# Performance work log

Hardware: AMD Instinct MI355X
Metric: run time of the kernel (lower is better)

The kernel has to match this reference:

```python
import jax, jax.numpy as jnp
import numpy as np

B, H = 4096, 200
NU, NV = 100000, 100000
DU, DV = 64, 64


def setup_inputs() -> dict:
    key = jax.random.key(0)
    ks = jax.random.split(key, 16)
    s = 0.05
    return {
        "nodes": jax.random.randint(ks[0], (B,), 0, NU),
        "history_uv": jax.random.randint(ks[1], (B, H), 0, NV),
        "history_r": jax.random.uniform(ks[2], (B, H), dtype=jnp.float32),
        "u2e_w": jax.random.normal(ks[3], (NU, DU), dtype=jnp.float32) * s,
        "v2e_w": jax.random.normal(ks[4], (NV, DV), dtype=jnp.float32) * s,
        "w_r1_w": jax.random.normal(ks[5], (DV, DV + 1), dtype=jnp.float32) * s,
        "w_r1_b": jax.random.normal(ks[6], (DV,), dtype=jnp.float32) * s,
        "w_r2_w": jax.random.normal(ks[7], (DV, DV), dtype=jnp.float32) * s,
        "w_r2_b": jax.random.normal(ks[8], (DV,), dtype=jnp.float32) * s,
        "att1_w": jax.random.normal(ks[9], (DV, DV + DU), dtype=jnp.float32) * s,
        "att1_b": jax.random.normal(ks[10], (DV,), dtype=jnp.float32) * s,
        "att2_w": jax.random.normal(ks[11], (DV, DV), dtype=jnp.float32) * s,
        "att2_b": jax.random.normal(ks[12], (DV,), dtype=jnp.float32) * s,
        "att3_w": jax.random.normal(ks[13], (1, DV), dtype=jnp.float32) * s,
        "att3_b": jax.random.normal(ks[14], (1,), dtype=jnp.float32) * s,
    }


def reference(nodes, history_uv, history_r, u2e_w, v2e_w,
              w_r1_w, w_r1_b, w_r2_w, w_r2_b,
              att1_w, att1_b, att2_w, att2_b, att3_w, att3_b):
    # Gather: e_uv [B,H,DV], uv_rep [B,DU]
    e_uv = v2e_w[history_uv]
    uv_rep = u2e_w[nodes]
    # x = cat(e_uv, e_r) -> two Linear+ReLU (dropout is identity in eval)
    x = jnp.concatenate([e_uv, history_r[..., None]], axis=-1)  # [B,H,DV+1]
    x = jax.nn.relu(jnp.einsum('bhi,oi->bho', x, w_r1_w) + w_r1_b)
    o_history = jax.nn.relu(jnp.einsum('bhi,oi->bho', x, w_r2_w) + w_r2_b)  # [B,H,DV]
    # Attention MLP over cat(o_history, u_rep broadcast to neighbors)
    u_rep_b = jnp.broadcast_to(uv_rep[:, None, :], (o_history.shape[0], o_history.shape[1], uv_rep.shape[-1]))
    a = jnp.concatenate([o_history, u_rep_b], axis=-1)  # [B,H,DV+DU]
    a = jax.nn.relu(jnp.einsum('bhi,oi->bho', a, att1_w) + att1_b)
    a = jax.nn.relu(jnp.einsum('bhi,oi->bho', a, att2_w) + att2_b)
    logits = jnp.einsum('bhi,oi->bho', a, att3_w) + att3_b  # [B,H,1]
    att = jax.nn.softmax(logits, axis=1)  # softmax over neighbor axis
    # Attention-weighted neighbor sum: [B,DV]
    to_feats = jnp.sum(o_history * att, axis=1)
    return to_feats
```

## Files before the change

kernel.cpp:

```cpp
#include <hip/hip_runtime.h>
#include <hip/hip_bf16.h>
#include <math.h>

#define Bn 4096
#define Hn 200

typedef float f32x16 __attribute__((ext_vector_type(16)));
typedef short short8 __attribute__((ext_vector_type(8)));
typedef __bf16 bh8 __attribute__((ext_vector_type(8)));
typedef unsigned int u32;

#define TABW     3200000
#define BIAS_OFF 10240
#define WR_OFF   10496
#define AT3_OFF  10560
#define WTOT     10624

__device__ __forceinline__ u32 pk2(float a, float b){
    union { __hip_bfloat162 bf; u32 u; } cv;
    cv.bf = __float22bfloat162_rn(make_float2(a, b));
    return cv.u;
}

template <typename T>
__device__ __forceinline__ auto mfma_sel(T a, T b, f32x16 c, int)
    -> decltype(__builtin_amdgcn_mfma_f32_32x32x16_bf16(a, b, c, 0, 0, 0)) {
    return __builtin_amdgcn_mfma_f32_32x32x16_bf16(a, b, c, 0, 0, 0);
}
template <typename T>
__device__ __forceinline__ f32x16 mfma_sel(T a, T b, f32x16 c, long) {
    return __builtin_amdgcn_mfma_f32_32x32x16_bf16(
        __builtin_bit_cast(bh8, a), __builtin_bit_cast(bh8, b), c, 0, 0, 0);
}
__device__ __forceinline__ f32x16 mfma_u4(uint4 a, uint4 b, f32x16 c){
    return mfma_sel(__builtin_bit_cast(short8, a), __builtin_bit_cast(short8, b), c, 0);
}

__device__ __forceinline__ void dtile_to_b(f32x16 d, uint4& b0, uint4& b1){
    u32 p0 = pk2(d[0], d[1]),   p1 = pk2(d[2], d[3]);
    u32 p2 = pk2(d[4], d[5]),   p3 = pk2(d[6], d[7]);
    u32 p4 = pk2(d[8], d[9]),   p5 = pk2(d[10], d[11]);
    u32 p6 = pk2(d[12], d[13]), p7 = pk2(d[14], d[15]);
    auto r0 = __builtin_amdgcn_permlane32_swap(p0, p2, false, false);
    auto r1 = __builtin_amdgcn_permlane32_swap(p1, p3, false, false);
    auto r2 = __builtin_amdgcn_permlane32_swap(p4, p6, false, false);
    auto r3 = __builtin_amdgcn_permlane32_swap(p5, p7, false, false);
    b0 = make_uint4((u32)r0[0], (u32)r1[0], (u32)r0[1], (u32)r1[1]);
    b1 = make_uint4((u32)r2[0], (u32)r3[0], (u32)r2[1], (u32)r3[1]);
}

__global__ __launch_bounds__(256) void prep(
    const float* __restrict__ v2e_w,
    const float* __restrict__ w_r1_w, const float* __restrict__ w_r1_b,
    const float* __restrict__ w_r2_w, const float* __restrict__ w_r2_b,
    const float* __restrict__ att1_w, const float* __restrict__ att1_b,
    const float* __restrict__ att2_w, const float* __restrict__ att2_b,
    const float* __restrict__ att3_w,
    u32* __restrict__ ws, int table_n, int woff)
{
    const int g = blockIdx.x * 256 + threadIdx.x;
    if (g < table_n) {
        const float4* src = (const float4*)v2e_w + (size_t)g * 2;
        float4 a = src[0], b = src[1];
        uint4 o; o.x = pk2(a.x, a.y); o.y = pk2(a.z, a.w);
                 o.z = pk2(b.x, b.y); o.w = pk2(b.z, b.w);
        ((uint4*)ws)[g] = o;
        return;
    }
    int q = g - table_n;
    u32* wbase = ws + woff;
    if (q < 2560) {
        const int c = q >> 6, l = q & 63, lo = l & 31, h = l >> 5;
        const float* W; int ldw, ft, kc, colb;
        if (c < 8)       { W = w_r1_w; ldw = 65;  ft = c >> 2;       kc = c & 3;       colb = 0; }
        else if (c < 16) { W = w_r2_w; ldw = 64;  ft = (c - 8) >> 2; kc = (c - 8) & 3; colb = 0; }
        else if (c < 32) { int c3 = c - 16; W = att1_w; ldw = 128; ft = c3 >> 3; kc = c3 & 3; colb = 64 * ((c3 >> 2) & 1); }
        else             { int c4 = c - 32; W = att2_w; ldw = 64;  ft = c4 >> 2; kc = c4 & 3; colb = 0; }
        const float* p = W + (32 * ft + lo) * ldw + colb + 16 * kc + 8 * h;
        uint4 o; o.x = pk2(p[0], p[1]); o.y = pk2(p[2], p[3]);
                 o.z = pk2(p[4], p[5]); o.w = pk2(p[6], p[7]);
        ((uint4*)wbase)[c * 64 + l] = o;
        return;
    }
    q -= 2560;
    if (q < 256) {
        const int layer = q >> 6, ft = (q >> 5) & 1, h = (q >> 4) & 1, rg = q & 15;
        const float* bp = layer == 0 ? w_r1_b : layer == 1 ? w_r2_b : layer == 2 ? att1_b : att2_b;
        ((float*)wbase)[BIAS_OFF + q] = bp[32 * ft + (rg & 3) + 8 * (rg >> 2) + 4 * h];
        return;
    }
    q -= 256;
    if (q < 64) {
        const int ft = (q >> 5) & 1, h = (q >> 4) & 1, rg = q & 15;
        ((float*)wbase)[WR_OFF + q] = w_r1_w[(32 * ft + (rg & 3) + 8 * (rg >> 2) + 4 * h) * 65 + 64];
        return;
    }
    q -= 64;
    if (q < 64) {
        const int ft = (q >> 5) & 1, h = (q >> 4) & 1, rg = q & 15;
        ((float*)wbase)[AT3_OFF + q] = att3_w[32 * ft + (rg & 3) + 8 * (rg >> 2) + 4 * h];
    }
}

template<int USE_TAB>
__global__ __launch_bounds__(256, 4) void uv_agg(
    const int* __restrict__ nodes,
    const int* __restrict__ history_uv,
    const float* __restrict__ history_r,
    const float* __restrict__ u2e_w,
    const float* __restrict__ v2e_w,
    const float* __restrict__ att3_b,
    const u32* __restrict__ ws,
    float* __restrict__ out)
{
    const int b  = blockIdx.x;
    const int t  = threadIdx.x;
    const int w  = t >> 6;
    const int l  = t & 63;
    const int lo = l & 31;
    const int h  = l >> 5;

    constexpr int woff = USE_TAB ? TABW : 0;
    const uint4* WF = (const uint4*)(ws + woff);
    const float* F  = (const float*)(ws + woff);

    __shared__ u32   oh_lds[Hn * 32];
    __shared__ float att_lds[256];
    __shared__ float red[4][64];
    __shared__ float swax[4], ssum[4];
    __shared__ u32   u_lds[32];

    if (t < 32) {
        const float2 uv = ((const float2*)(u2e_w + (size_t)nodes[b] * 64))[t];
        u_lds[t] = pk2(uv.x, uv.y);
    }

    const int hb  = b * Hn;
    const int m0  = 64 * w + lo;
    const int m1  = m0 + 32;
    const int mi0 = m0 < Hn ? m0 : Hn - 1;
    const int mi1 = m1 < Hn ? m1 : Hn - 1;
    const int vidx0 = history_uv[hb + mi0];
    const int vidx1 = history_uv[hb + mi1];
    const float rv[2] = { history_r[hb + mi0], history_r[hb + mi1] };

    uint4 eB[2][4];
    if constexpr (USE_TAB) {
        const uint4* t0 = (const uint4*)ws + (size_t)vidx0 * 8;
        const uint4* t1 = (const uint4*)ws + (size_t)vidx1 * 8;
#pragma unroll
        for (int kc = 0; kc < 4; ++kc){ eB[0][kc] = t0[2*kc + h]; eB[1][kc] = t1[2*kc + h]; }
    } else {
        const float4* p0 = (const float4*)(v2e_w + (size_t)vidx0 * 64);
        const float4* p1 = (const float4*)(v2e_w + (size_t)vidx1 * 64);
#pragma unroll
        for (int kc = 0; kc < 4; ++kc){
            float4 a = p0[4*kc + 2*h], c = p0[4*kc + 2*h + 1];
            eB[0][kc] = make_uint4(pk2(a.x, a.y), pk2(a.z, a.w), pk2(c.x, c.y), pk2(c.z, c.w));
            a = p1[4*kc + 2*h]; c = p1[4*kc + 2*h + 1];
            eB[1][kc] = make_uint4(pk2(a.x, a.y), pk2(a.z, a.w), pk2(c.x, c.y), pk2(c.z, c.w));
        }
    }

    uint4 x1B[2][4];
#pragma unroll
    for (int ft = 0; ft < 2; ++ft){
        uint4 W[4];
#pragma unroll
        for (int kc = 0; kc < 4; ++kc) W[kc] = WF[(ft*4 + kc)*64 + l];
        const float4* bp = (const float4*)(F + BIAS_OFF + ft*32 + h*16);
        const float4* wp = (const float4*)(F + WR_OFF  + ft*32 + h*16);
#pragma unroll
        for (int rt = 0; rt < 2; ++rt){
            f32x16 a;
#pragma unroll
            for (int i = 0; i < 4; ++i){
                float4 bv = bp[i], wv = wp[i];
                a[4*i+0] = fmaf(wv.x, rv[rt], bv.x); a[4*i+1] = fmaf(wv.y, rv[rt], bv.y);
                a[4*i+2] = fmaf(wv.z, rv[rt], bv.z); a[4*i+3] = fmaf(wv.w, rv[rt], bv.w);
            }
#pragma unroll
            for (int kc = 0; kc < 4; ++kc) a = mfma_u4(W[kc], eB[rt][kc], a);
#pragma unroll
            for (int i = 0; i < 16; ++i) a[i] = fmaxf(a[i], 0.f);
            dtile_to_b(a, x1B[rt][2*ft], x1B[rt][2*ft+1]);
        }
    }

    uint4 ohB[2][4];
#pragma unroll
    for (int ft = 0; ft < 2; ++ft){
        uint4 W[4];
#pragma unroll
        for (int kc = 0; kc < 4; ++kc) W[kc] = WF[(8 + ft*4 + kc)*64 + l];
        const float4* bp = (const float4*)(F + BIAS_OFF + 64 + ft*32 + h*16);
#pragma unroll
        for (int rt = 0; rt < 2; ++rt){
            f32x16 a;
#pragma unroll
            for (int i = 0; i < 4; ++i){
                float4 bv = bp[i];
                a[4*i+0] = bv.x; a[4*i+1] = bv.y; a[4*i+2] = bv.z; a[4*i+3] = bv.w;
            }
#pragma unroll
            for (int kc = 0; kc < 4; ++kc) a = mfma_u4(W[kc], x1B[rt][kc], a);
#pragma unroll
            for (int i = 0; i < 16; ++i) a[i] = fmaxf(a[i], 0.f);
            dtile_to_b(a, ohB[rt][2*ft], ohB[rt][2*ft+1]);
        }
    }

#pragma unroll
    for (int rt = 0; rt < 2; ++rt){
        const int m = 64 * w + 32 * rt + lo;
        if (m < Hn) {
#pragma unroll
            for (int kc = 0; kc < 4; ++kc){
                const u32* pw = (const u32*)&ohB[rt][kc];
#pragma unroll
                for (int v = 0; v < 4; ++v){
                    const int c = 8 * kc + 4 * h + v;
                    oh_lds[m * 32 + (c ^ lo)] = pw[v];
                }
            }
        }
    }

    __syncthreads();

    uint4 a1B[2][4];
#pragma unroll
    for (int ft = 0; ft < 2; ++ft){
        uint4 W[4];
#pragma unroll
        for (int kc = 0; kc < 4; ++kc) W[kc] = WF[(16 + ft*8 + kc)*64 + l];
        const float4* bp = (const float4*)(F + BIAS_OFF + 128 + ft*32 + h*16);
        f32x16 a[2];
#pragma unroll
        for (int rt = 0; rt < 2; ++rt){
#pragma unroll
            for (int i = 0; i < 4; ++i){
                float4 bv = bp[i];
                a[rt][4*i+0] = bv.x; a[rt][4*i+1] = bv.y; a[rt][4*i+2] = bv.z; a[rt][4*i+3] = bv.w;
            }
#pragma unroll
            for (int kc = 0; kc < 4; ++kc) a[rt] = mfma_u4(W[kc], ohB[rt][kc], a[rt]);
        }
#pragma unroll
        for (int kc = 0; kc < 4; ++kc){
            uint4 W2 = WF[(16 + ft*8 + 4 + kc)*64 + l];
            uint4 uu = *(const uint4*)&u_lds[8*kc + 4*h];
#pragma unroll
            for (int rt = 0; rt < 2; ++rt) a[rt] = mfma_u4(W2, uu, a[rt]);
        }
#pragma unroll
        for (int rt = 0; rt < 2; ++rt){
#pragma unroll
            for (int i = 0; i < 16; ++i) a[rt][i] = fmaxf(a[rt][i], 0.f);
            dtile_to_b(a[rt], a1B[rt][2*ft], a1B[rt][2*ft+1]);
        }
    }

    float lgp[2] = {0.f, 0.f};
#pragma unroll
    for (int ft = 0; ft < 2; ++ft){
        uint4 W[4];
#pragma unroll
        for (int kc = 0; kc < 4; ++kc) W[kc] = WF[(32 + ft*4 + kc)*64 + l];
        const float4* bp = (const float4*)(F + BIAS_OFF + 192 + ft*32 + h*16);
        const float4* ap = (const float4*)(F + AT3_OFF + ft*32 + h*16);
#pragma unroll
        for (int rt = 0; rt < 2; ++rt){
            f32x16 a;
#pragma unroll
            for (int i = 0; i < 4; ++i){
                float4 bv = bp[i];
                a[4*i+0] = bv.x; a[4*i+1] = bv.y; a[4*i+2] = bv.z; a[4*i+3] = bv.w;
            }
#pragma unroll
            for (int kc = 0; kc < 4; ++kc) a = mfma_u4(W[kc], a1B[rt][kc], a);
#pragma unroll
            for (int i = 0; i < 4; ++i){
                float4 av = ap[i];
                lgp[rt] = fmaf(fmaxf(a[4*i+0], 0.f), av.x, lgp[rt]);
                lgp[rt] = fmaf(fmaxf(a[4*i+1], 0.f), av.y, lgp[rt]);
                lgp[rt] = fmaf(fmaxf(a[4*i+2], 0.f), av.z, lgp[rt]);
                lgp[rt] = fmaf(fmaxf(a[4*i+3], 0.f), av.w, lgp[rt]);
            }
        }
    }
    const float b3 = att3_b[0];
    float lg0 = lgp[0] + __shfl_xor(lgp[0], 32, 64) + b3;
    float lg1 = lgp[1] + __shfl_xor(lgp[1], 32, 64) + b3;
    if (m0 >= Hn) lg0 = -1e30f;
    if (m1 >= Hn) lg1 = -1e30f;

    float mx = fmaxf(lg0, lg1);
#pragma unroll
    for (int d = 16; d >= 1; d >>= 1) mx = fmaxf(mx, __shfl_xor(mx, d, 64));
    if (l == 0) swax[w] = mx;
    __syncthreads();
    mx = fmaxf(fmaxf(swax[0], swax[1]), fmaxf(swax[2], swax[3]));
    const float e0 = exp2f((lg0 - mx) * 1.4426950408889634f);
    const float e1 = exp2f((lg1 - mx) * 1.4426950408889634f);
    float sm = e0 + e1;
#pragma unroll
    for (int d = 16; d >= 1; d >>= 1) sm += __shfl_xor(sm, d, 64);
    if (l == 0) ssum[w] = sm;
    __syncthreads();
    const float inv = 1.f / (ssum[0] + ssum[1] + ssum[2] + ssum[3]);
    att_lds[64 * w + 32 * h + lo] = (h ? e1 : e0) * inv;
    __syncthreads();

    float s0 = 0.f, s1 = 0.f;
#pragma unroll 8
    for (int i = 0; i < 32; ++i){
        const int row = 64 * w + 32 * h + i;
        const int ri  = row < Hn ? row : Hn - 1;
        const u32 wv  = oh_lds[ri * 32 + (lo ^ (ri & 31))];
        const float av = att_lds[row];
        s0 = fmaf(__uint_as_float(wv << 16), av, s0);
        s1 = fmaf(__uint_as_float(wv & 0xffff0000u), av, s1);
    }
    s0 += __shfl_xor(s0, 32, 64);
    s1 += __shfl_xor(s1, 32, 64);
    if (l < 32){ red[w][2 * lo] = s0; red[w][2 * lo + 1] = s1; }
    __syncthreads();
    if (t < 64)
        out[b * 64 + t] = red[0][t] + red[1][t] + red[2][t] + red[3][t];
}

extern "C" void kernel_launch(void* const* d_in, const int* in_sizes, int n_in,
                              void* d_out, int out_size, void* d_ws, size_t ws_size,
                              hipStream_t stream) {
    u32* ws = (u32*)d_ws;
    const size_t need_tab = (size_t)(TABW + WTOT) * 4;
    const int use_tab = (ws_size >= need_tab) ? 1 : 0;
    const int woff    = use_tab ? TABW : 0;
    const int table_n = use_tab ? 800000 : 0;
    const int prep_threads = table_n + 2944;
    const int prep_blocks  = (prep_threads + 255) / 256;

    prep<<<prep_blocks, 256, 0, stream>>>(
        (const float*)d_in[4],
        (const float*)d_in[5],  (const float*)d_in[6],
        (const float*)d_in[7],  (const float*)d_in[8],
        (const float*)d_in[9],  (const float*)d_in[10],
        (const float*)d_in[11], (const float*)d_in[12],
        (const float*)d_in[13],
        ws, table_n, woff);

    if (use_tab) {
        uv_agg<1><<<Bn, 256, 0, stream>>>(
            (const int*)d_in[0], (const int*)d_in[1], (const float*)d_in[2],
            (const float*)d_in[3], (const float*)d_in[4], (const float*)d_in[14],
            ws, (float*)d_out);
    } else {
        uv_agg<0><<<Bn, 256, 0, stream>>>(
            (const int*)d_in[0], (const int*)d_in[1], (const float*)d_in[2],
            (const float*)d_in[3], (const float*)d_in[4], (const float*)d_in[14],
            ws, (float*)d_out);
    }
}
```

Baseline: 90.45 us.

## Skip padded row tile in last wave and hoist user-embedding MFMA

Wave 3 covers rows 192-255, but only 192-199 are real, so its second 32-row tile is pure padding. That wave now skips the second gather and every MFMA chain for that tile, and masks its logits. The user-embedding half of att1 is now computed once per feature tile and reused for both row tiles, rather than being accumulated separately for each. o_history is no longer kept in registers: it is written to LDS with 64-bit stores under a new XOR swizzle and read back for att1, which adds LDS traffic and changes the bank-conflict pattern.

```diff
diff --git a/kernel.cpp b/kernel.cpp
--- a/kernel.cpp
+++ b/kernel.cpp
@@ -124,7 +124,7 @@
     const uint4* WF = (const uint4*)(ws + woff);
     const float* F  = (const float*)(ws + woff);
 
-    __shared__ u32   oh_lds[Hn * 32];
+    __shared__ u32   oh_lds[224 * 32];
     __shared__ float att_lds[256];
     __shared__ float red[4][64];
     __shared__ float swax[4], ssum[4];
@@ -134,6 +134,8 @@
         const float2 uv = ((const float2*)(u2e_w + (size_t)nodes[b] * 64))[t];
         u_lds[t] = pk2(uv.x, uv.y);
     }
+
+    const bool full = (w != 3);
 
     const int hb  = b * Hn;
     const int m0  = 64 * w + lo;
@@ -141,24 +143,34 @@
     const int mi0 = m0 < Hn ? m0 : Hn - 1;
     const int mi1 = m1 < Hn ? m1 : Hn - 1;
     const int vidx0 = history_uv[hb + mi0];
-    const int vidx1 = history_uv[hb + mi1];
-    const float rv[2] = { history_r[hb + mi0], history_r[hb + mi1] };
+    float rv[2];
+    rv[0] = history_r[hb + mi0];
+    rv[1] = history_r[hb + mi1];
 
     uint4 eB[2][4];
     if constexpr (USE_TAB) {
         const uint4* t0 = (const uint4*)ws + (size_t)vidx0 * 8;
-        const uint4* t1 = (const uint4*)ws + (size_t)vidx1 * 8;
-#pragma unroll
-        for (int kc = 0; kc < 4; ++kc){ eB[0][kc] = t0[2*kc + h]; eB[1][kc] = t1[2*kc + h]; }
+#pragma unroll
+        for (int kc = 0; kc < 4; ++kc) eB[0][kc] = t0[2*kc + h];
+        if (full) {
+            const uint4* t1 = (const uint4*)ws + (size_t)history_uv[hb + mi1] * 8;
+#pragma unroll
+            for (int kc = 0; kc < 4; ++kc) eB[1][kc] = t1[2*kc + h];
+        }
     } else {
         const float4* p0 = (const float4*)(v2e_w + (size_t)vidx0 * 64);
-        const float4* p1 = (const float4*)(v2e_w + (size_t)vidx1 * 64);
 #pragma unroll
         for (int kc = 0; kc < 4; ++kc){
             float4 a = p0[4*kc + 2*h], c = p0[4*kc + 2*h + 1];
             eB[0][kc] = make_uint4(pk2(a.x, a.y), pk2(a.z, a.w), pk2(c.x, c.y), pk2(c.z, c.w));
-            a = p1[4*kc + 2*h]; c = p1[4*kc + 2*h + 1];
-            eB[1][kc] = make_uint4(pk2(a.x, a.y), pk2(a.z, a.w), pk2(c.x, c.y), pk2(c.z, c.w));
+        }
+        if (full) {
+            const float4* p1 = (const float4*)(v2e_w + (size_t)history_uv[hb + mi1] * 64);
+#pragma unroll
+            for (int kc = 0; kc < 4; ++kc){
+                float4 a = p1[4*kc + 2*h], c = p1[4*kc + 2*h + 1];
+                eB[1][kc] = make_uint4(pk2(a.x, a.y), pk2(a.z, a.w), pk2(c.x, c.y), pk2(c.z, c.w));
+            }
         }
     }
 
@@ -172,22 +184,23 @@
         const float4* wp = (const float4*)(F + WR_OFF  + ft*32 + h*16);
 #pragma unroll
         for (int rt = 0; rt < 2; ++rt){
-            f32x16 a;
-#pragma unroll
-            for (int i = 0; i < 4; ++i){
-                float4 bv = bp[i], wv = wp[i];
-                a[4*i+0] = fmaf(wv.x, rv[rt], bv.x); a[4*i+1] = fmaf(wv.y, rv[rt], bv.y);
-                a[4*i+2] = fmaf(wv.z, rv[rt], bv.z); a[4*i+3] = fmaf(wv.w, rv[rt], bv.w);
-            }
-#pragma unroll
-            for (int kc = 0; kc < 4; ++kc) a = mfma_u4(W[kc], eB[rt][kc], a);
-#pragma unroll
-            for (int i = 0; i < 16; ++i) a[i] = fmaxf(a[i], 0.f);
-            dtile_to_b(a, x1B[rt][2*ft], x1B[rt][2*ft+1]);
-        }
-    }
-
-    uint4 ohB[2][4];
+            if (rt == 0 || full) {
+                f32x16 a;
+#pragma unroll
+                for (int i = 0; i < 4; ++i){
+                    float4 bv = bp[i], wv = wp[i];
+                    a[4*i+0] = fmaf(wv.x, rv[rt], bv.x); a[4*i+1] = fmaf(wv.y, rv[rt], bv.y);
+                    a[4*i+2] = fmaf(wv.z, rv[rt], bv.z); a[4*i+3] = fmaf(wv.w, rv[rt], bv.w);
+                }
+#pragma unroll
+                for (int kc = 0; kc < 4; ++kc) a = mfma_u4(W[kc], eB[rt][kc], a);
+#pragma unroll
+                for (int i = 0; i < 16; ++i) a[i] = fmaxf(a[i], 0.f);
+                dtile_to_b(a, x1B[rt][2*ft], x1B[rt][2*ft+1]);
+            }
+        }
+    }
+
 #pragma unroll
     for (int ft = 0; ft < 2; ++ft){
         uint4 W[4];
@@ -196,68 +209,80 @@
         const float4* bp = (const float4*)(F + BIAS_OFF + 64 + ft*32 + h*16);
 #pragma unroll
         for (int rt = 0; rt < 2; ++rt){
-            f32x16 a;
+            if (rt == 0 || full) {
+                f32x16 a;
+#pragma unroll
+                for (int i = 0; i < 4; ++i){
+                    float4 bv = bp[i];
+                    a[4*i+0] = bv.x; a[4*i+1] = bv.y; a[4*i+2] = bv.z; a[4*i+3] = bv.w;
+                }
+#pragma unroll
+                for (int kc = 0; kc < 4; ++kc) a = mfma_u4(W[kc], x1B[rt][kc], a);
+#pragma unroll
+                for (int i = 0; i < 16; ++i) a[i] = fmaxf(a[i], 0.f);
+                uint4 b0, b1;
+                dtile_to_b(a, b0, b1);
+                const int m = 64 * w + 32 * rt + lo;
+                if (m < Hn) {
+                    uint2* oh2 = (uint2*)oh_lds;
+                    const int x  = (lo & 15) << 1;
+                    const int q0 = (16*ft + 4*h) ^ x;
+                    const int base = m * 16;
+                    oh2[base + ( q0      >> 1)] = make_uint2(b0.x, b0.y);
+                    oh2[base + ((q0 ^ 2) >> 1)] = make_uint2(b0.z, b0.w);
+                    oh2[base + ((q0 ^ 8) >> 1)] = make_uint2(b1.x, b1.y);
+                    oh2[base + ((q0 ^10) >> 1)] = make_uint2(b1.z, b1.w);
+                }
+            }
+        }
+    }
+
+    __syncthreads();
+
+    uint4 a1B[2][4];
+#pragma unroll
+    for (int ft = 0; ft < 2; ++ft){
+        f32x16 accu;
+        {
+            uint4 Wu[4];
+#pragma unroll
+            for (int kc = 0; kc < 4; ++kc) Wu[kc] = WF[(16 + ft*8 + 4 + kc)*64 + l];
+            const float4* bp = (const float4*)(F + BIAS_OFF + 128 + ft*32 + h*16);
 #pragma unroll
             for (int i = 0; i < 4; ++i){
                 float4 bv = bp[i];
-                a[4*i+0] = bv.x; a[4*i+1] = bv.y; a[4*i+2] = bv.z; a[4*i+3] = bv.w;
-            }
-#pragma unroll
-            for (int kc = 0; kc < 4; ++kc) a = mfma_u4(W[kc], x1B[rt][kc], a);
-#pragma unroll
-            for (int i = 0; i < 16; ++i) a[i] = fmaxf(a[i], 0.f);
-            dtile_to_b(a, ohB[rt][2*ft], ohB[rt][2*ft+1]);
-        }
-    }
-
-#pragma unroll
-    for (int rt = 0; rt < 2; ++rt){
-        const int m = 64 * w + 32 * rt + lo;
-        if (m < Hn) {
+                accu[4*i+0] = bv.x; accu[4*i+1] = bv.y; accu[4*i+2] = bv.z; accu[4*i+3] = bv.w;
+            }
 #pragma unroll
             for (int kc = 0; kc < 4; ++kc){
-                const u32* pw = (const u32*)&ohB[rt][kc];
-#pragma unroll
-                for (int v = 0; v < 4; ++v){
-                    const int c = 8 * kc + 4 * h + v;
-                    oh_lds[m * 32 + (c ^ lo)] = pw[v];
-                }
-            }
-        }
-    }
-
-    __syncthreads();
-
-    uint4 a1B[2][4];
-#pragma unroll
-    for (int ft = 0; ft < 2; ++ft){
-        uint4 W[4];
-#pragma unroll
-        for (int kc = 0; kc < 4; ++kc) W[kc] = WF[(16 + ft*8 + kc)*64 + l];
-        const float4* bp = (const float4*)(F + BIAS_OFF + 128 + ft*32 + h*16);
-        f32x16 a[2];
+                uint4 uu = *(const uint4*)&u_lds[8*kc + 4*h];
+                accu = mfma_u4(Wu[kc], uu, accu);
+            }
+        }
+        uint4 Wo[4];
+#pragma unroll
+        for (int kc = 0; kc < 4; ++kc) Wo[kc] = WF[(16 + ft*8 + kc)*64 + l];
 #pragma unroll
         for (int rt = 0; rt < 2; ++rt){
-#pragma unroll
-            for (int i = 0; i < 4; ++i){
-                float4 bv = bp[i];
-                a[rt][4*i+0] = bv.x; a[rt][4*i+1] = bv.y; a[rt][4*i+2] = bv.z; a[rt][4*i+3] = bv.w;
-            }
-#pragma unroll
-            for (int kc = 0; kc < 4; ++kc) a[rt] = mfma_u4(W[kc], ohB[rt][kc], a[rt]);
-        }
-#pragma unroll
-        for (int kc = 0; kc < 4; ++kc){
-            uint4 W2 = WF[(16 + ft*8 + 4 + kc)*64 + l];
-            uint4 uu = *(const uint4*)&u_lds[8*kc + 4*h];
-#pragma unroll
-            for (int rt = 0; rt < 2; ++rt) a[rt] = mfma_u4(W2, uu, a[rt]);
-        }
-#pragma unroll
-        for (int rt = 0; rt < 2; ++rt){
-#pragma unroll
-            for (int i = 0; i < 16; ++i) a[rt][i] = fmaxf(a[rt][i], 0.f);
-            dtile_to_b(a[rt], a1B[rt][2*ft], a1B[rt][2*ft+1]);
+            if (rt == 0 || full) {
+                const int m = 64 * w + 32 * rt + lo;
+                const int x = (lo & 15) << 1;
+                const uint2* oh2 = (const uint2*)oh_lds;
+                uint4 frag[4];
+#pragma unroll
+                for (int kc = 0; kc < 4; ++kc){
+                    const int q = (8*kc + 4*h) ^ x;
+                    uint2 ra = oh2[m*16 + ( q      >> 1)];
+                    uint2 rb = oh2[m*16 + ((q ^ 2) >> 1)];
+                    frag[kc] = make_uint4(ra.x, ra.y, rb.x, rb.y);
+                }
+                f32x16 a = accu;
+#pragma unroll
+                for (int kc = 0; kc < 4; ++kc) a = mfma_u4(Wo[kc], frag[kc], a);
+#pragma unroll
+                for (int i = 0; i < 16; ++i) a[i] = fmaxf(a[i], 0.f);
+                dtile_to_b(a, a1B[rt][2*ft], a1B[rt][2*ft+1]);
+            }
         }
     }
 
@@ -271,21 +296,23 @@
         const float4* ap = (const float4*)(F + AT3_OFF + ft*32 + h*16);
 #pragma unroll
         for (int rt = 0; rt < 2; ++rt){
-            f32x16 a;
-#pragma unroll
-            for (int i = 0; i < 4; ++i){
-                float4 bv = bp[i];
-                a[4*i+0] = bv.x; a[4*i+1] = bv.y; a[4*i+2] = bv.z; a[4*i+3] = bv.w;
-            }
-#pragma unroll
-            for (int kc = 0; kc < 4; ++kc) a = mfma_u4(W[kc], a1B[rt][kc], a);
-#pragma unroll
-            for (int i = 0; i < 4; ++i){
-                float4 av = ap[i];
-                lgp[rt] = fmaf(fmaxf(a[4*i+0], 0.f), av.x, lgp[rt]);
-                lgp[rt] = fmaf(fmaxf(a[4*i+1], 0.f), av.y, lgp[rt]);
-                lgp[rt] = fmaf(fmaxf(a[4*i+2], 0.f), av.z, lgp[rt]);
-                lgp[rt] = fmaf(fmaxf(a[4*i+3], 0.f), av.w, lgp[rt]);
+            if (rt == 0 || full) {
+                f32x16 a;
+#pragma unroll
+                for (int i = 0; i < 4; ++i){
+                    float4 bv = bp[i];
+                    a[4*i+0] = bv.x; a[4*i+1] = bv.y; a[4*i+2] = bv.z; a[4*i+3] = bv.w;
+                }
+#pragma unroll
+                for (int kc = 0; kc < 4; ++kc) a = mfma_u4(W[kc], a1B[rt][kc], a);
+#pragma unroll
+                for (int i = 0; i < 4; ++i){
+                    float4 av = ap[i];
+                    lgp[rt] = fmaf(fmaxf(a[4*i+0], 0.f), av.x, lgp[rt]);
+                    lgp[rt] = fmaf(fmaxf(a[4*i+1], 0.f), av.y, lgp[rt]);
+                    lgp[rt] = fmaf(fmaxf(a[4*i+2], 0.f), av.z, lgp[rt]);
+                    lgp[rt] = fmaf(fmaxf(a[4*i+3], 0.f), av.w, lgp[rt]);
+                }
             }
         }
     }
@@ -293,7 +320,7 @@
     float lg0 = lgp[0] + __shfl_xor(lgp[0], 32, 64) + b3;
     float lg1 = lgp[1] + __shfl_xor(lgp[1], 32, 64) + b3;
     if (m0 >= Hn) lg0 = -1e30f;
-    if (m1 >= Hn) lg1 = -1e30f;
+    if (m1 >= Hn || !full) lg1 = -1e30f;
 
     float mx = fmaxf(lg0, lg1);
 #pragma unroll
@@ -317,7 +344,7 @@
     for (int i = 0; i < 32; ++i){
         const int row = 64 * w + 32 * h + i;
         const int ri  = row < Hn ? row : Hn - 1;
-        const u32 wv  = oh_lds[ri * 32 + (lo ^ (ri & 31))];
+        const u32 wv  = oh_lds[ri * 32 + (lo ^ ((ri & 15) << 1))];
         const float av = att_lds[row];
         s0 = fmaf(__uint_as_float(wv << 16), av, s0);
         s1 = fmaf(__uint_as_float(wv & 0xffff0000u), av, s1);
```

New measurement: 84.36 us. 6.7% less time.
